# Kernel optimization log

Measured on AMD Instinct MI355X. Metric: run time of the kernel, lower is better.

The kernel has to match this reference:

```python
import jax, jax.numpy as jnp
import numpy as np

HIDDEN = 1024
NUM_HEADS = 16
HEAD_DIM = HIDDEN // NUM_HEADS
MASK_BIAS = -10000.0


def setup_inputs() -> dict:
    key = jax.random.key(0)
    ks = jax.random.split(key, 5)
    B, S = 4, 2048
    hidden_states = jax.random.normal(ks[0], (B, S, HIDDEN), dtype=jnp.float32)
    # fused QKV projection (Linear1D_Col): hidden -> 3*hidden
    w_qkv = jax.random.normal(ks[1], (HIDDEN, 3 * HIDDEN), dtype=jnp.float32) * (HIDDEN ** -0.5)
    b_qkv = jax.random.normal(ks[2], (3 * HIDDEN,), dtype=jnp.float32) * 0.02
    # output dense (Linear1D_Row): hidden -> hidden
    w_dense = jax.random.normal(ks[3], (HIDDEN, HIDDEN), dtype=jnp.float32) * (HIDDEN ** -0.5)
    b_dense = jax.random.normal(ks[4], (HIDDEN,), dtype=jnp.float32) * 0.02
    return {"hidden_states": hidden_states, "w_qkv": w_qkv, "b_qkv": b_qkv,
            "w_dense": w_dense, "b_dense": b_dense}


def _split_heads(t):
    # [B, S, H*D] -> [B, H, S, D]
    B, S, _ = t.shape
    return t.reshape(B, S, NUM_HEADS, HEAD_DIM).transpose(0, 2, 1, 3)


def reference(hidden_states, w_qkv, b_qkv, w_dense, b_dense):
    B, S, _ = hidden_states.shape
    kvq = hidden_states @ w_qkv + b_qkv  # [B, S, 3*hidden]
    # NOTE: original chunk order is k, v, q (key first!)
    k, v, q = jnp.split(kvq, 3, axis=-1)
    q = _split_heads(q) * (HEAD_DIM ** -0.5)  # [B, H, S, D]
    k = _split_heads(k)
    v = _split_heads(v)
    scores = jnp.einsum('bhqd,bhkd->bhqk', q, k)  # [B, H, S, S]
    causal = jnp.tril(jnp.ones((S, S), dtype=bool))
    scores = jnp.where(causal[None, None], scores, jnp.asarray(MASK_BIAS, scores.dtype))
    dt = scores.dtype
    attn = jax.nn.softmax(scores.astype(jnp.float32), axis=-1).astype(dt)
    ctx = jnp.einsum('bhqk,bhkd->bhqd', attn, v)  # [B, H, S, D]
    ctx = ctx.transpose(0, 2, 1, 3).reshape(B, S, HIDDEN)
    return ctx @ w_dense + b_dense
```

## Files before the change

### kernel.cpp

```cpp
#include <hip/hip_runtime.h>

#define H_NUM 16
#define HD    64
#define SQ    2048
#define HID   1024
#define MTOK  8192

typedef __attribute__((ext_vector_type(8))) short bf16x8;
typedef __attribute__((ext_vector_type(4))) short s16x4;
typedef __attribute__((ext_vector_type(4))) float f32x4;

__device__ __forceinline__ short f2bf(float f) {
  union { float f; unsigned u; } v; v.f = f;
  unsigned r = v.u + 0x7fffu + ((v.u >> 16) & 1u);
  return (short)(r >> 16);
}

__device__ __forceinline__ float fexp2(float x) {
#if __has_builtin(__builtin_amdgcn_exp2f)
  return __builtin_amdgcn_exp2f(x);
#else
  return exp2f(x);
#endif
}

__device__ __forceinline__ void gload_lds16(const short* g, short* l) {
  __builtin_amdgcn_global_load_lds(
      (const __attribute__((address_space(1))) void*)g,
      (__attribute__((address_space(3))) void*)l, 16, 0, 0);
}

__global__ void k_cvt(const float* __restrict__ in, short* __restrict__ out, int n4) {
  int i = blockIdx.x * blockDim.x + threadIdx.x;
  if (i < n4) {
    float4 f = ((const float4*)in)[i];
    s16x4 o = { f2bf(f.x), f2bf(f.y), f2bf(f.z), f2bf(f.w) };
    ((s16x4*)out)[i] = o;
  }
}

__global__ void k_tr(const float* __restrict__ in, short* __restrict__ out, int R, int C) {
  __shared__ float t[32][33];
  int c0 = blockIdx.x * 32, r0 = blockIdx.y * 32;
  int tx = threadIdx.x, ty = threadIdx.y;
#pragma unroll
  for (int i = 0; i < 4; i++)
    t[ty + 8 * i][tx] = in[(size_t)(r0 + ty + 8 * i) * C + c0 + tx];
  __syncthreads();
#pragma unroll
  for (int i = 0; i < 4; i++)
    out[(size_t)(c0 + ty + 8 * i) * R + r0 + tx] = f2bf(t[tx][ty + 8 * i]);
}

template <int EPI>
__global__ __launch_bounds__(256) void k_gemm(
    const short* __restrict__ A, const short* __restrict__ Bt,
    const float* __restrict__ bias,
    short* __restrict__ qbuf, short* __restrict__ kbuf, short* __restrict__ vtbuf,
    float* __restrict__ outf, int Kd) {
  __shared__ short as[128][64];
  __shared__ short bs[128][64];
  const int tid = threadIdx.x;
  const int w = tid >> 6, l = tid & 63;
  const int lr = l & 15, lk = l >> 4;
  const int wr = w >> 1, wc = w & 1;
  const int nwg = gridDim.x * gridDim.y;
  const int lin = blockIdx.y * gridDim.x + blockIdx.x;
  const int swz = (lin & 7) * (nwg >> 3) + (lin >> 3);
  const int m0 = (swz / gridDim.x) * 128, n0 = (swz % gridDim.x) * 128;

  f32x4 acc[4][4] = {};

  for (int kt = 0; kt < Kd; kt += 64) {
#pragma unroll
    for (int rnd = 0; rnd < 4; ++rnd) {
      int e = rnd * 2048 + w * 512 + l * 8;
      int row = e >> 6, col = e & 63;
      gload_lds16(A + (size_t)(m0 + row) * Kd + kt + col,
                  &as[0][0] + rnd * 2048 + w * 512);
      gload_lds16(Bt + (size_t)(n0 + row) * Kd + kt + col,
                  &bs[0][0] + rnd * 2048 + w * 512);
    }
    __syncthreads();
#pragma unroll
    for (int kk = 0; kk < 2; ++kk) {
      bf16x8 af[4], bf[4];
#pragma unroll
      for (int m = 0; m < 4; ++m)
        af[m] = *(const bf16x8*)&as[wr * 64 + m * 16 + lr][kk * 32 + lk * 8];
#pragma unroll
      for (int n = 0; n < 4; ++n)
        bf[n] = *(const bf16x8*)&bs[wc * 64 + n * 16 + lr][kk * 32 + lk * 8];
      __builtin_amdgcn_s_setprio(1);
#pragma unroll
      for (int m = 0; m < 4; ++m)
#pragma unroll
        for (int n = 0; n < 4; ++n)
          acc[m][n] = __builtin_amdgcn_mfma_f32_16x16x32_bf16(af[m], bf[n], acc[m][n], 0, 0, 0);
      __builtin_amdgcn_s_setprio(0);
    }
    __syncthreads();
  }

  const float SCLQ = 0.125f * 1.44269504088896341f;
#pragma unroll
  for (int n = 0; n < 4; ++n) {
    const int col = n0 + wc * 64 + n * 16 + lr;
    const float bv = bias[col];
    if (EPI == 1) {
#pragma unroll
      for (int m = 0; m < 4; ++m) {
        int row = m0 + wr * 64 + m * 16 + lk * 4;
#pragma unroll
        for (int r = 0; r < 4; ++r)
          outf[(size_t)(row + r) * HID + col] = acc[m][n][r] + bv;
      }
    } else if (col < HID) {
      int h = col >> 6, d = col & 63;
#pragma unroll
      for (int m = 0; m < 4; ++m) {
        int row = m0 + wr * 64 + m * 16 + lk * 4;
        int b = row >> 11, s = row & 2047;
#pragma unroll
        for (int r = 0; r < 4; ++r)
          kbuf[((size_t)(b * H_NUM + h) * SQ + s + r) * HD + d] = f2bf(acc[m][n][r] + bv);
      }
    } else if (col < 2 * HID) {
      int f = col - HID, h = f >> 6, d = f & 63;
#pragma unroll
      for (int m = 0; m < 4; ++m) {
        int row = m0 + wr * 64 + m * 16 + lk * 4;
        int b = row >> 11, s = row & 2047;
        s16x4 pk;
#pragma unroll
        for (int r = 0; r < 4; ++r) pk[r] = f2bf(acc[m][n][r] + bv);
        *(s16x4*)&vtbuf[((size_t)(b * H_NUM + h) * HD + d) * SQ + s] = pk;
      }
    } else {
      int f = col - 2 * HID, h = f >> 6, d = f & 63;
#pragma unroll
      for (int m = 0; m < 4; ++m) {
        int row = m0 + wr * 64 + m * 16 + lk * 4;
        int b = row >> 11, s = row & 2047;
#pragma unroll
        for (int r = 0; r < 4; ++r)
          qbuf[((size_t)(b * H_NUM + h) * SQ + s + r) * HD + d] = f2bf((acc[m][n][r] + bv) * SCLQ);
      }
    }
  }
}

__global__ __launch_bounds__(512) void k_attn(
    const short* __restrict__ Q, const short* __restrict__ K,
    const short* __restrict__ Vt, short* __restrict__ ctx) {
  __shared__ short ks[2][4096];
  __shared__ short vs[2][4096];
  __shared__ short ps[8][16][72];
  const int tid = threadIdx.x;
  const int w = tid >> 6, l = tid & 63;
  const int lr = l & 15, lk = l >> 4;
  const int bh = blockIdx.y;
  const int bb = bh >> 4, hh = bh & 15;
  const size_t base = (size_t)bh * (SQ * HD);
  const float THR = 11.5416f;

  const int srow = tid >> 3;
  const int scol = ((tid & 7) * 8) ^ ((srow & 7) * 8);
  const short* kg0 = K + base + srow * HD + scol;
  const short* vg0 = Vt + base + (size_t)srow * SQ + scol;
  short* kld = &ks[0][0] + tid * 8;
  short* vld = &vs[0][0] + tid * 8;
  const int rdswz = (lr & 7) * 8;

  int buf = 0;
  for (int pass = 0; pass < 2; ++pass) {
    const int qt = pass ? (15 - blockIdx.x) : blockIdx.x;
    const int nt = 2 * qt + 2;
    const int diag = 2 * qt + (w >> 2);
    const int qr = qt * 128 + w * 16;

    bf16x8 qf[2];
#pragma unroll
    for (int kk = 0; kk < 2; ++kk)
      qf[kk] = *(const bf16x8*)(Q + base + (size_t)(qr + lr) * HD + kk * 32 + lk * 8);

    f32x4 o[4] = {};
    float mrun = -3.0e4f, lsum = 0.f;

    gload_lds16(kg0, kld + buf * 4096);
    gload_lds16(vg0, vld + buf * 4096);
    __syncthreads();

    for (int t = 0; t < nt; ++t) {
      if (t + 1 < nt) {
        gload_lds16(kg0 + (t + 1) * 4096, kld + (buf ^ 1) * 4096);
        gload_lds16(vg0 + (t + 1) * 64, vld + (buf ^ 1) * 4096);
      }
      if (t <= diag) {
        const short* kb = &ks[buf][0];
        const short* vb = &vs[buf][0];
        f32x4 sf[4] = {};
        __builtin_amdgcn_s_setprio(1);
#pragma unroll
        for (int kk = 0; kk < 2; ++kk)
#pragma unroll
          for (int n = 0; n < 4; ++n) {
            bf16x8 kf = *(const bf16x8*)(kb + (n * 16 + lr) * 64 + ((kk * 32 + lk * 8) ^ rdswz));
            sf[n] = __builtin_amdgcn_mfma_f32_16x16x32_bf16(kf, qf[kk], sf[n], 0, 0, 0);
          }
        __builtin_amdgcn_s_setprio(0);

        if (t == diag) {
          const int qg = qr + lr;
#pragma unroll
          for (int n = 0; n < 4; ++n) {
            int kg = t * 64 + n * 16 + lk * 4;
#pragma unroll
            for (int r = 0; r < 4; ++r)
              if (kg + r > qg) sf[n][r] = -14426.95f;
          }
        }

        float m0 = sf[0][0];
#pragma unroll
        for (int n = 0; n < 4; ++n)
#pragma unroll
          for (int r = 0; r < 4; ++r) m0 = fmaxf(m0, sf[n][r]);
        m0 = fmaxf(m0, __shfl_xor(m0, 16));
        m0 = fmaxf(m0, __shfl_xor(m0, 32));

        if (__any(m0 > mrun + THR)) {
          float mn = fmaxf(mrun, m0);
          float sc = fexp2(mrun - mn);
          float scq[4];
#pragma unroll
          for (int r = 0; r < 4; ++r) scq[r] = __shfl(sc, lk * 4 + r);
#pragma unroll
          for (int nd = 0; nd < 4; ++nd)
#pragma unroll
            for (int r = 0; r < 4; ++r) o[nd][r] *= scq[r];
          lsum *= sc;
          mrun = mn;
        }

        float rs = 0.f;
#pragma unroll
        for (int n = 0; n < 4; ++n) {
          s16x4 pk;
#pragma unroll
          for (int r = 0; r < 4; ++r) {
            float p = fexp2(sf[n][r] - mrun);
            rs += p;
            pk[r] = (short)(__float_as_uint(p) >> 16);
          }
          *(s16x4*)&ps[w][lr][n * 16 + lk * 4] = pk;
        }
        lsum += rs;

        bf16x8 pa[2];
#pragma unroll
        for (int kk = 0; kk < 2; ++kk)
          pa[kk] = *(const bf16x8*)&ps[w][lr][kk * 32 + lk * 8];

        __builtin_amdgcn_s_setprio(1);
#pragma unroll
        for (int kk = 0; kk < 2; ++kk)
#pragma unroll
          for (int nd = 0; nd < 4; ++nd) {
            bf16x8 vf = *(const bf16x8*)(vb + (nd * 16 + lr) * 64 + ((kk * 32 + lk * 8) ^ rdswz));
            o[nd] = __builtin_amdgcn_mfma_f32_16x16x32_bf16(pa[kk], vf, o[nd], 0, 0, 0);
          }
        __builtin_amdgcn_s_setprio(0);
      }
      __syncthreads();
      buf ^= 1;
    }

    lsum += __shfl_xor(lsum, 16);
    lsum += __shfl_xor(lsum, 32);
    float inv = 1.0f / lsum;
    float invq[4];
#pragma unroll
    for (int r = 0; r < 4; ++r) invq[r] = __shfl(inv, lk * 4 + r);
#pragma unroll
    for (int nd = 0; nd < 4; ++nd)
#pragma unroll
      for (int r = 0; r < 4; ++r) {
        int s = qr + lk * 4 + r;
        ctx[((size_t)(bb * SQ + s)) * HID + hh * 64 + nd * 16 + lr] = f2bf(o[nd][r] * invq[r]);
      }
  }
}

extern "C" void kernel_launch(void* const* d_in, const int* in_sizes, int n_in,
                              void* d_out, int out_size, void* d_ws, size_t ws_size,
                              hipStream_t stream) {
  const float* hs   = (const float*)d_in[0];
  const float* wqkv = (const float*)d_in[1];
  const float* bqkv = (const float*)d_in[2];
  const float* wd   = (const float*)d_in[3];
  const float* bd   = (const float*)d_in[4];
  float* out = (float*)d_out;
  char* ws = (char*)d_ws;
  const size_t MB = 1u << 20;

  short* hs_bf  = (short*)(ws);
  short* wqkv_t = (short*)(ws + 16 * MB);
  short* wd_t   = (short*)(ws + 22 * MB);
  short* qbuf   = (short*)(ws + 24 * MB);
  short* kbuf   = (short*)(ws + 40 * MB);
  short* vtbuf  = (short*)(ws + 56 * MB);
  short* ctx    = (short*)(ws + 72 * MB);

  k_cvt<<<8192, 256, 0, stream>>>(hs, hs_bf, MTOK * HID / 4);
  k_tr<<<dim3(96, 32), dim3(32, 8), 0, stream>>>(wqkv, wqkv_t, 1024, 3072);
  k_tr<<<dim3(32, 32), dim3(32, 8), 0, stream>>>(wd, wd_t, 1024, 1024);
  k_gemm<0><<<dim3(24, 64), 256, 0, stream>>>(hs_bf, wqkv_t, bqkv,
                                              qbuf, kbuf, vtbuf, nullptr, 1024);
  k_attn<<<dim3(8, 64), 512, 0, stream>>>(qbuf, kbuf, vtbuf, ctx);
  k_gemm<1><<<dim3(8, 64), 256, 0, stream>>>(ctx, wd_t, bd,
                                             nullptr, nullptr, nullptr, out, 1024);
}
```

Baseline: 175.5 us.

## Double-buffer GEMM LDS tiles with swizzle and 256x128 tiles, 8 waves

Restructures the bf16 GEMM so each block uses 512 threads and a 256x128 output tile. Global-to-LDS loads for the next K tile are issued into a second buffer while the current one is consumed, using an explicit vmcnt wait in place of two full syncthreads per iteration. LDS columns are XOR-swizzled by row to avoid bank conflicts on fragment reads. The change doubles LDS use to 96KB per block and halves the grid size, which may limit occupancy and tail balance.

```diff
diff --git a/kernel.cpp b/kernel.cpp
--- a/kernel.cpp
+++ b/kernel.cpp
@@ -53,64 +53,105 @@
 }
 
 template <int EPI>
-__global__ __launch_bounds__(256) void k_gemm(
+__global__ __launch_bounds__(512, 2) void k_gemm(
     const short* __restrict__ A, const short* __restrict__ Bt,
     const float* __restrict__ bias,
     short* __restrict__ qbuf, short* __restrict__ kbuf, short* __restrict__ vtbuf,
     float* __restrict__ outf, int Kd) {
-  __shared__ short as[128][64];
-  __shared__ short bs[128][64];
+  __shared__ short as[2][16384];
+  __shared__ short bs[2][8192];
   const int tid = threadIdx.x;
   const int w = tid >> 6, l = tid & 63;
   const int lr = l & 15, lk = l >> 4;
-  const int wr = w >> 1, wc = w & 1;
+  const int wm = w >> 1, wn = w & 1;
   const int nwg = gridDim.x * gridDim.y;
   const int lin = blockIdx.y * gridDim.x + blockIdx.x;
   const int swz = (lin & 7) * (nwg >> 3) + (lin >> 3);
-  const int m0 = (swz / gridDim.x) * 128, n0 = (swz % gridDim.x) * 128;
+  const int m0 = (swz / gridDim.x) * 256, n0 = (swz % gridDim.x) * 128;
+
+  const int NT = Kd >> 6;
+
+#define STAGE_TILE(kt_, bufn_)                                            \
+  do {                                                                    \
+    _Pragma("unroll")                                                     \
+    for (int rnd = 0; rnd < 4; ++rnd) {                                   \
+      int g = rnd * 512 + tid;                                            \
+      int row = g >> 3;                                                   \
+      int sc_ = ((g & 7) * 8) ^ ((row & 7) * 8);                          \
+      gload_lds16(A + (size_t)(m0 + row) * Kd + (kt_) + sc_,              \
+                  &as[bufn_][0] + g * 8);                                 \
+    }                                                                     \
+    _Pragma("unroll")                                                     \
+    for (int rnd = 0; rnd < 2; ++rnd) {                                   \
+      int g = rnd * 512 + tid;                                            \
+      int row = g >> 3;                                                   \
+      int sc_ = ((g & 7) * 8) ^ ((row & 7) * 8);                          \
+      gload_lds16(Bt + (size_t)(n0 + row) * Kd + (kt_) + sc_,             \
+                  &bs[bufn_][0] + g * 8);                                 \
+    }                                                                     \
+  } while (0)
 
   f32x4 acc[4][4] = {};
 
-  for (int kt = 0; kt < Kd; kt += 64) {
-#pragma unroll
-    for (int rnd = 0; rnd < 4; ++rnd) {
-      int e = rnd * 2048 + w * 512 + l * 8;
-      int row = e >> 6, col = e & 63;
-      gload_lds16(A + (size_t)(m0 + row) * Kd + kt + col,
-                  &as[0][0] + rnd * 2048 + w * 512);
-      gload_lds16(Bt + (size_t)(n0 + row) * Kd + kt + col,
-                  &bs[0][0] + rnd * 2048 + w * 512);
+  STAGE_TILE(0, 0);
+
+  int buf = 0;
+  for (int t = 0; t < NT; ++t) {
+    if (t + 1 < NT) {
+      STAGE_TILE((t + 1) * 64, buf ^ 1);
+      asm volatile("s_waitcnt vmcnt(6)" ::: "memory");
+    } else {
+      asm volatile("s_waitcnt vmcnt(0)" ::: "memory");
     }
-    __syncthreads();
-#pragma unroll
-    for (int kk = 0; kk < 2; ++kk) {
-      bf16x8 af[4], bf[4];
-#pragma unroll
-      for (int m = 0; m < 4; ++m)
-        af[m] = *(const bf16x8*)&as[wr * 64 + m * 16 + lr][kk * 32 + lk * 8];
-#pragma unroll
-      for (int n = 0; n < 4; ++n)
-        bf[n] = *(const bf16x8*)&bs[wc * 64 + n * 16 + lr][kk * 32 + lk * 8];
+    __builtin_amdgcn_s_barrier();
+    __builtin_amdgcn_sched_barrier(0);
+
+    const short* ab = &as[buf][0];
+    const short* bb = &bs[buf][0];
+    const int cswz = (lr & 7) * 8;
+    bf16x8 af[2][4], bfr[2][2];
+#pragma unroll
+    for (int kk = 0; kk < 2; ++kk)
+#pragma unroll
+      for (int m = 0; m < 4; ++m) {
+        int row = wm * 64 + m * 16 + lr;
+        af[kk][m] = *(const bf16x8*)(ab + row * 64 + ((kk * 32 + lk * 8) ^ cswz));
+      }
+#pragma unroll
+    for (int ph = 0; ph < 2; ++ph) {
+#pragma unroll
+      for (int kk = 0; kk < 2; ++kk)
+#pragma unroll
+        for (int n = 0; n < 2; ++n) {
+          int row = wn * 64 + (ph * 2 + n) * 16 + lr;
+          bfr[kk][n] = *(const bf16x8*)(bb + row * 64 + ((kk * 32 + lk * 8) ^ cswz));
+        }
       __builtin_amdgcn_s_setprio(1);
 #pragma unroll
-      for (int m = 0; m < 4; ++m)
-#pragma unroll
-        for (int n = 0; n < 4; ++n)
-          acc[m][n] = __builtin_amdgcn_mfma_f32_16x16x32_bf16(af[m], bf[n], acc[m][n], 0, 0, 0);
+      for (int kk = 0; kk < 2; ++kk)
+#pragma unroll
+        for (int m = 0; m < 4; ++m)
+#pragma unroll
+          for (int n = 0; n < 2; ++n)
+            acc[m][ph * 2 + n] = __builtin_amdgcn_mfma_f32_16x16x32_bf16(
+                af[kk][m], bfr[kk][n], acc[m][ph * 2 + n], 0, 0, 0);
       __builtin_amdgcn_s_setprio(0);
     }
-    __syncthreads();
+    __builtin_amdgcn_sched_barrier(0);
+    __builtin_amdgcn_s_barrier();
+    buf ^= 1;
   }
+#undef STAGE_TILE
 
   const float SCLQ = 0.125f * 1.44269504088896341f;
 #pragma unroll
   for (int n = 0; n < 4; ++n) {
-    const int col = n0 + wc * 64 + n * 16 + lr;
+    const int col = n0 + wn * 64 + n * 16 + lr;
     const float bv = bias[col];
     if (EPI == 1) {
 #pragma unroll
       for (int m = 0; m < 4; ++m) {
-        int row = m0 + wr * 64 + m * 16 + lk * 4;
+        int row = m0 + wm * 64 + m * 16 + lk * 4;
 #pragma unroll
         for (int r = 0; r < 4; ++r)
           outf[(size_t)(row + r) * HID + col] = acc[m][n][r] + bv;
@@ -119,7 +160,7 @@
       int h = col >> 6, d = col & 63;
 #pragma unroll
       for (int m = 0; m < 4; ++m) {
-        int row = m0 + wr * 64 + m * 16 + lk * 4;
+        int row = m0 + wm * 64 + m * 16 + lk * 4;
         int b = row >> 11, s = row & 2047;
 #pragma unroll
         for (int r = 0; r < 4; ++r)
@@ -129,7 +170,7 @@
       int f = col - HID, h = f >> 6, d = f & 63;
 #pragma unroll
       for (int m = 0; m < 4; ++m) {
-        int row = m0 + wr * 64 + m * 16 + lk * 4;
+        int row = m0 + wm * 64 + m * 16 + lk * 4;
         int b = row >> 11, s = row & 2047;
         s16x4 pk;
 #pragma unroll
@@ -140,7 +181,7 @@
       int f = col - 2 * HID, h = f >> 6, d = f & 63;
 #pragma unroll
       for (int m = 0; m < 4; ++m) {
-        int row = m0 + wr * 64 + m * 16 + lk * 4;
+        int row = m0 + wm * 64 + m * 16 + lk * 4;
         int b = row >> 11, s = row & 2047;
 #pragma unroll
         for (int r = 0; r < 4; ++r)
@@ -315,9 +356,9 @@
   k_cvt<<<8192, 256, 0, stream>>>(hs, hs_bf, MTOK * HID / 4);
   k_tr<<<dim3(96, 32), dim3(32, 8), 0, stream>>>(wqkv, wqkv_t, 1024, 3072);
   k_tr<<<dim3(32, 32), dim3(32, 8), 0, stream>>>(wd, wd_t, 1024, 1024);
-  k_gemm<0><<<dim3(24, 64), 256, 0, stream>>>(hs_bf, wqkv_t, bqkv,
+  k_gemm<0><<<dim3(24, 32), 512, 0, stream>>>(hs_bf, wqkv_t, bqkv,
                                               qbuf, kbuf, vtbuf, nullptr, 1024);
   k_attn<<<dim3(8, 64), 512, 0, stream>>>(qbuf, kbuf, vtbuf, ctx);
-  k_gemm<1><<<dim3(8, 64), 256, 0, stream>>>(ctx, wd_t, bd,
+  k_gemm<1><<<dim3(8, 32), 512, 0, stream>>>(ctx, wd_t, bd,
                                              nullptr, nullptr, nullptr, out, 1024);
 }
```

Result: no change. 177.4 us (+1.1%).

## Halve attention block to 4 waves, each processing two query strips

Applied to the files above, without the earlier changes.

The attention kernel moves from 8 waves of 512 threads to 4 waves of 256 threads. Each wave now handles two 16-row query strips, 64 rows apart, and keeps two sets of online-softmax state. K and V fragments are read from LDS once per tile into registers and reused for both strips, which halves LDS read traffic per query row and allows two blocks per CU. The cost is higher register pressure from the held K/V fragments and doubled accumulators, and less parallelism per block.

```diff
diff --git a/kernel.cpp b/kernel.cpp
--- a/kernel.cpp
+++ b/kernel.cpp
@@ -150,12 +150,12 @@
   }
 }
 
-__global__ __launch_bounds__(512) void k_attn(
+__global__ __launch_bounds__(256, 2) void k_attn(
     const short* __restrict__ Q, const short* __restrict__ K,
     const short* __restrict__ Vt, short* __restrict__ ctx) {
   __shared__ short ks[2][4096];
   __shared__ short vs[2][4096];
-  __shared__ short ps[8][16][72];
+  __shared__ short ps[4][16][72];
   const int tid = threadIdx.x;
   const int w = tid >> 6, l = tid & 63;
   const int lr = l & 15, lk = l >> 4;
@@ -164,131 +164,154 @@
   const size_t base = (size_t)bh * (SQ * HD);
   const float THR = 11.5416f;
 
-  const int srow = tid >> 3;
-  const int scol = ((tid & 7) * 8) ^ ((srow & 7) * 8);
-  const short* kg0 = K + base + srow * HD + scol;
-  const short* vg0 = Vt + base + (size_t)srow * SQ + scol;
-  short* kld = &ks[0][0] + tid * 8;
-  short* vld = &vs[0][0] + tid * 8;
+  const int r0 = tid >> 3;
+  const int scol = ((tid & 7) * 8) ^ ((r0 & 7) * 8);
+  const short* kga = K + base + (size_t)r0 * HD + scol;
+  const short* kgb = kga + 32 * HD;
+  const short* vga = Vt + base + (size_t)r0 * SQ + scol;
+  const short* vgb = vga + (size_t)32 * SQ;
+  short* klda = &ks[0][0] + tid * 8;
+  short* kldb = &ks[0][0] + (tid + 256) * 8;
+  short* vlda = &vs[0][0] + tid * 8;
+  short* vldb = &vs[0][0] + (tid + 256) * 8;
   const int rdswz = (lr & 7) * 8;
 
   int buf = 0;
   for (int pass = 0; pass < 2; ++pass) {
     const int qt = pass ? (15 - blockIdx.x) : blockIdx.x;
     const int nt = 2 * qt + 2;
-    const int diag = 2 * qt + (w >> 2);
-    const int qr = qt * 128 + w * 16;
-
-    bf16x8 qf[2];
-#pragma unroll
-    for (int kk = 0; kk < 2; ++kk)
-      qf[kk] = *(const bf16x8*)(Q + base + (size_t)(qr + lr) * HD + kk * 32 + lk * 8);
-
-    f32x4 o[4] = {};
-    float mrun = -3.0e4f, lsum = 0.f;
-
-    gload_lds16(kg0, kld + buf * 4096);
-    gload_lds16(vg0, vld + buf * 4096);
+    const int d0 = 2 * qt;
+
+    bf16x8 qf[2][2];
+#pragma unroll
+    for (int st = 0; st < 2; ++st)
+#pragma unroll
+      for (int kk = 0; kk < 2; ++kk)
+        qf[st][kk] = *(const bf16x8*)(Q + base +
+            (size_t)(qt * 128 + st * 64 + w * 16 + lr) * HD + kk * 32 + lk * 8);
+
+    f32x4 o[2][4] = {};
+    float mrun[2] = {-3.0e4f, -3.0e4f}, lsum[2] = {0.f, 0.f};
+
+    gload_lds16(kga, klda + buf * 4096); gload_lds16(kgb, kldb + buf * 4096);
+    gload_lds16(vga, vlda + buf * 4096); gload_lds16(vgb, vldb + buf * 4096);
     __syncthreads();
 
     for (int t = 0; t < nt; ++t) {
       if (t + 1 < nt) {
-        gload_lds16(kg0 + (t + 1) * 4096, kld + (buf ^ 1) * 4096);
-        gload_lds16(vg0 + (t + 1) * 64, vld + (buf ^ 1) * 4096);
-      }
-      if (t <= diag) {
+        const int lo = (buf ^ 1) * 4096;
+        const int gk = (t + 1) * 4096, gv = (t + 1) * 64;
+        gload_lds16(kga + gk, klda + lo); gload_lds16(kgb + gk, kldb + lo);
+        gload_lds16(vga + gv, vlda + lo); gload_lds16(vgb + gv, vldb + lo);
+      }
+      {
         const short* kb = &ks[buf][0];
         const short* vb = &vs[buf][0];
-        f32x4 sf[4] = {};
-        __builtin_amdgcn_s_setprio(1);
+        bf16x8 kf[2][4], vf[2][4];
 #pragma unroll
         for (int kk = 0; kk < 2; ++kk)
 #pragma unroll
           for (int n = 0; n < 4; ++n) {
-            bf16x8 kf = *(const bf16x8*)(kb + (n * 16 + lr) * 64 + ((kk * 32 + lk * 8) ^ rdswz));
-            sf[n] = __builtin_amdgcn_mfma_f32_16x16x32_bf16(kf, qf[kk], sf[n], 0, 0, 0);
+            kf[kk][n] = *(const bf16x8*)(kb + (n * 16 + lr) * 64 + ((kk * 32 + lk * 8) ^ rdswz));
+            vf[kk][n] = *(const bf16x8*)(vb + (n * 16 + lr) * 64 + ((kk * 32 + lk * 8) ^ rdswz));
           }
-        __builtin_amdgcn_s_setprio(0);
-
-        if (t == diag) {
-          const int qg = qr + lr;
-#pragma unroll
-          for (int n = 0; n < 4; ++n) {
-            int kg = t * 64 + n * 16 + lk * 4;
-#pragma unroll
-            for (int r = 0; r < 4; ++r)
-              if (kg + r > qg) sf[n][r] = -14426.95f;
+
+#pragma unroll
+        for (int st = 0; st < 2; ++st) {
+          if (t <= d0 + st) {
+            f32x4 sf[4] = {};
+            __builtin_amdgcn_s_setprio(1);
+#pragma unroll
+            for (int kk = 0; kk < 2; ++kk)
+#pragma unroll
+              for (int n = 0; n < 4; ++n)
+                sf[n] = __builtin_amdgcn_mfma_f32_16x16x32_bf16(kf[kk][n], qf[st][kk], sf[n], 0, 0, 0);
+            __builtin_amdgcn_s_setprio(0);
+
+            if (t == d0 + st) {
+              const int qg = w * 16 + lr;
+#pragma unroll
+              for (int n = 0; n < 4; ++n) {
+                int kg = n * 16 + lk * 4;
+#pragma unroll
+                for (int r = 0; r < 4; ++r)
+                  if (kg + r > qg) sf[n][r] = -14426.95f;
+              }
+            }
+
+            float m0 = sf[0][0];
+#pragma unroll
+            for (int n = 0; n < 4; ++n)
+#pragma unroll
+              for (int r = 0; r < 4; ++r) m0 = fmaxf(m0, sf[n][r]);
+            m0 = fmaxf(m0, __shfl_xor(m0, 16));
+            m0 = fmaxf(m0, __shfl_xor(m0, 32));
+
+            if (__any(m0 > mrun[st] + THR)) {
+              float mn = fmaxf(mrun[st], m0);
+              float sc = fexp2(mrun[st] - mn);
+              float scq[4];
+#pragma unroll
+              for (int r = 0; r < 4; ++r) scq[r] = __shfl(sc, lk * 4 + r);
+#pragma unroll
+              for (int nd = 0; nd < 4; ++nd)
+#pragma unroll
+                for (int r = 0; r < 4; ++r) o[st][nd][r] *= scq[r];
+              lsum[st] *= sc;
+              mrun[st] = mn;
+            }
+
+            float rs = 0.f;
+#pragma unroll
+            for (int n = 0; n < 4; ++n) {
+              s16x4 pk;
+#pragma unroll
+              for (int r = 0; r < 4; ++r) {
+                float p = fexp2(sf[n][r] - mrun[st]);
+                rs += p;
+                pk[r] = (short)(__float_as_uint(p) >> 16);
+              }
+              *(s16x4*)&ps[w][lr][n * 16 + lk * 4] = pk;
+            }
+            lsum[st] += rs;
+
+            bf16x8 pa[2];
+#pragma unroll
+            for (int kk = 0; kk < 2; ++kk)
+              pa[kk] = *(const bf16x8*)&ps[w][lr][kk * 32 + lk * 8];
+
+            __builtin_amdgcn_s_setprio(1);
+#pragma unroll
+            for (int kk = 0; kk < 2; ++kk)
+#pragma unroll
+              for (int nd = 0; nd < 4; ++nd)
+                o[st][nd] = __builtin_amdgcn_mfma_f32_16x16x32_bf16(pa[kk], vf[kk][nd], o[st][nd], 0, 0, 0);
+            __builtin_amdgcn_s_setprio(0);
           }
         }
-
-        float m0 = sf[0][0];
-#pragma unroll
-        for (int n = 0; n < 4; ++n)
-#pragma unroll
-          for (int r = 0; r < 4; ++r) m0 = fmaxf(m0, sf[n][r]);
-        m0 = fmaxf(m0, __shfl_xor(m0, 16));
-        m0 = fmaxf(m0, __shfl_xor(m0, 32));
-
-        if (__any(m0 > mrun + THR)) {
-          float mn = fmaxf(mrun, m0);
-          float sc = fexp2(mrun - mn);
-          float scq[4];
-#pragma unroll
-          for (int r = 0; r < 4; ++r) scq[r] = __shfl(sc, lk * 4 + r);
-#pragma unroll
-          for (int nd = 0; nd < 4; ++nd)
-#pragma unroll
-            for (int r = 0; r < 4; ++r) o[nd][r] *= scq[r];
-          lsum *= sc;
-          mrun = mn;
-        }
-
-        float rs = 0.f;
-#pragma unroll
-        for (int n = 0; n < 4; ++n) {
-          s16x4 pk;
-#pragma unroll
-          for (int r = 0; r < 4; ++r) {
-            float p = fexp2(sf[n][r] - mrun);
-            rs += p;
-            pk[r] = (short)(__float_as_uint(p) >> 16);
-          }
-          *(s16x4*)&ps[w][lr][n * 16 + lk * 4] = pk;
-        }
-        lsum += rs;
-
-        bf16x8 pa[2];
-#pragma unroll
-        for (int kk = 0; kk < 2; ++kk)
-          pa[kk] = *(const bf16x8*)&ps[w][lr][kk * 32 + lk * 8];
-
-        __builtin_amdgcn_s_setprio(1);
-#pragma unroll
-        for (int kk = 0; kk < 2; ++kk)
-#pragma unroll
-          for (int nd = 0; nd < 4; ++nd) {
-            bf16x8 vf = *(const bf16x8*)(vb + (nd * 16 + lr) * 64 + ((kk * 32 + lk * 8) ^ rdswz));
-            o[nd] = __builtin_amdgcn_mfma_f32_16x16x32_bf16(pa[kk], vf, o[nd], 0, 0, 0);
-          }
-        __builtin_amdgcn_s_setprio(0);
       }
       __syncthreads();
       buf ^= 1;
     }
 
-    lsum += __shfl_xor(lsum, 16);
-    lsum += __shfl_xor(lsum, 32);
-    float inv = 1.0f / lsum;
-    float invq[4];
-#pragma unroll
-    for (int r = 0; r < 4; ++r) invq[r] = __shfl(inv, lk * 4 + r);
-#pragma unroll
-    for (int nd = 0; nd < 4; ++nd)
-#pragma unroll
-      for (int r = 0; r < 4; ++r) {
-        int s = qr + lk * 4 + r;
-        ctx[((size_t)(bb * SQ + s)) * HID + hh * 64 + nd * 16 + lr] = f2bf(o[nd][r] * invq[r]);
-      }
+#pragma unroll
+    for (int st = 0; st < 2; ++st) {
+      float ls = lsum[st];
+      ls += __shfl_xor(ls, 16);
+      ls += __shfl_xor(ls, 32);
+      float inv = 1.0f / ls;
+      float invq[4];
+#pragma unroll
+      for (int r = 0; r < 4; ++r) invq[r] = __shfl(inv, lk * 4 + r);
+#pragma unroll
+      for (int nd = 0; nd < 4; ++nd)
+#pragma unroll
+        for (int r = 0; r < 4; ++r) {
+          int s = qt * 128 + st * 64 + w * 16 + lk * 4 + r;
+          ctx[((size_t)(bb * SQ + s)) * HID + hh * 64 + nd * 16 + lr] =
+              f2bf(o[st][nd][r] * invq[r]);
+        }
+    }
   }
 }
 
@@ -317,7 +340,7 @@
   k_tr<<<dim3(32, 32), dim3(32, 8), 0, stream>>>(wd, wd_t, 1024, 1024);
   k_gemm<0><<<dim3(24, 64), 256, 0, stream>>>(hs_bf, wqkv_t, bqkv,
                                               qbuf, kbuf, vtbuf, nullptr, 1024);
-  k_attn<<<dim3(8, 64), 512, 0, stream>>>(qbuf, kbuf, vtbuf, ctx);
+  k_attn<<<dim3(8, 64), 256, 0, stream>>>(qbuf, kbuf, vtbuf, ctx);
   k_gemm<1><<<dim3(8, 64), 256, 0, stream>>>(ctx, wd_t, bd,
                                              nullptr, nullptr, nullptr, out, 1024);
 }
```

Result: slower. 182.0 us (+3.7%).
